# Kernel tuning notes

Measured on AMD Instinct MI355X. Metric: run time of the kernel, lower is better.

## Reference

```python
import jax, jax.numpy as jnp
import numpy as np

B, S, HIST = 2, 2048, 2048
H, HK, D = 16, 16, 128
DIM = H * D

def setup_inputs() -> dict:
    key = jax.random.key(0)
    ks = jax.random.split(key, 8)
    x = jax.random.normal(ks[0], (B, S, DIM), jnp.float32)
    prev_k = jax.random.normal(ks[1], (B, HIST, HK, D), jnp.float32)
    prev_v = jax.random.normal(ks[2], (B, HIST, HK, D), jnp.float32)
    # causal mask: history fully visible, causal within the current chunk
    q_pos = HIST + jnp.arange(S)
    k_pos = jnp.arange(HIST + S)
    mask = jnp.where(k_pos[None, :] <= q_pos[:, None], 0.0, -1e9).astype(jnp.float32)[None, None]
    sc = 0.02
    wq = jax.random.normal(ks[3], (DIM, DIM), jnp.float32) * sc
    wk = jax.random.normal(ks[4], (DIM, DIM), jnp.float32) * sc
    wv = jax.random.normal(ks[5], (DIM, DIM), jnp.float32) * sc
    wo = jax.random.normal(ks[6], (DIM, DIM), jnp.float32) * sc
    return {"x": x, "prev_k": prev_k, "prev_v": prev_v, "mask": mask,
            "wq": wq, "wk": wk, "wv": wv, "wo": wo}

def reference(x, prev_k, prev_v, mask, wq, wk, wv, wo):
    b, s, _ = x.shape
    # nn.Linear: y = x @ W^T, weights stored [out, in]
    xq = jnp.einsum('bsd,ed->bse', x, wq).reshape(b, s, H, D)
    xk = jnp.einsum('bsd,ed->bse', x, wk).reshape(b, s, HK, D)
    xv = jnp.einsum('bsd,ed->bse', x, wv).reshape(b, s, HK, D)
    k_all = jnp.concatenate([prev_k, xk], axis=1)  # [b, hist+s, hk, d]
    v_all = jnp.concatenate([prev_v, xv], axis=1)
    scores = jnp.einsum('bqhd,bkhd->bhqk', xq, k_all) / jnp.sqrt(jnp.float32(D))
    scores = scores + mask
    probs = jax.nn.softmax(scores.astype(jnp.float32), axis=-1).astype(xq.dtype)
    out = jnp.einsum('bhqk,bkhd->bqhd', probs, v_all).reshape(b, s, H * D)
    out = jnp.einsum('bse,de->bsd', out, wo)
    return out, k_all, v_all
```

## Files before the change

### kernel.cpp

```cpp
#include <hip/hip_runtime.h>
#include <math.h>

typedef __attribute__((ext_vector_type(8))) short bf16x8;
typedef __attribute__((ext_vector_type(4))) short bf16x4;
typedef __attribute__((ext_vector_type(4))) float f32x4;

#define SSCL (0.08838834764831845f * 1.4426950408889634f)

__device__ __forceinline__ short f2bf(float f) {
    union { float f; unsigned u; } x; x.f = f;
    unsigned r = x.u + 0x7fffu + ((x.u >> 16) & 1u);
    return (short)(r >> 16);
}

typedef const __attribute__((address_space(1))) unsigned int* gas_ptr;
typedef __attribute__((address_space(3))) unsigned int* las_ptr;
__device__ __forceinline__ void async_copy16(const void* g, void* l) {
    __builtin_amdgcn_global_load_lds((gas_ptr)g, (las_ptr)l, 16, 0, 0);
}

__global__ __launch_bounds__(256)
void cvt_kernel(const float* __restrict__ src, short* __restrict__ dst, int n4) {
    int i = blockIdx.x * 256 + threadIdx.x;
    const int stride = gridDim.x * 256;
    for (; i < n4; i += stride) {
        float4 v = ((const float4*)src)[i];
        bf16x4 o;
        o[0] = f2bf(v.x); o[1] = f2bf(v.y); o[2] = f2bf(v.z); o[3] = f2bf(v.w);
        ((bf16x4*)dst)[i] = o;
    }
}

__global__ __launch_bounds__(256)
void cvt3_kernel(const float* __restrict__ s0, const float* __restrict__ s1,
                 const float* __restrict__ s2, short* __restrict__ d0,
                 short* __restrict__ d1, short* __restrict__ d2, int n4) {
    const float* src = (blockIdx.y == 0) ? s0 : ((blockIdx.y == 1) ? s1 : s2);
    short* dst = (blockIdx.y == 0) ? d0 : ((blockIdx.y == 1) ? d1 : d2);
    int i = blockIdx.x * 256 + threadIdx.x;
    const int stride = gridDim.x * 256;
    for (; i < n4; i += stride) {
        float4 v = ((const float4*)src)[i];
        bf16x4 o;
        o[0] = f2bf(v.x); o[1] = f2bf(v.y); o[2] = f2bf(v.z); o[3] = f2bf(v.w);
        ((bf16x4*)dst)[i] = o;
    }
}

template<int QKV>
__global__ __launch_bounds__(256)
void gemm_kernel(const short* __restrict__ A,
                 const short* __restrict__ B0, const short* __restrict__ B1,
                 const short* __restrict__ B2,
                 short* __restrict__ D16, float* __restrict__ Dk,
                 float* __restrict__ Dv, float* __restrict__ Df) {
    __shared__ short As[128 * 64];
    __shared__ short Bs[128 * 64];
    const int tid = threadIdx.x, w = tid >> 6, ln = tid & 63;
    const int col = ln & 15, quad = ln >> 4;
    const int sel = QKV ? (blockIdx.x >> 4) : 0;
    const int tn = (blockIdx.x & 15) * 128;
    const int tm = blockIdx.y * 128;
    const short* B = (sel == 0) ? B0 : ((sel == 1) ? B1 : B2);

    const int wm = (w >> 1) * 64, wn = (w & 1) * 64;
    const int srow = ln >> 3, scol = (ln & 7) * 8;

    f32x4 acc[4][4];
    for (int i = 0; i < 4; ++i)
        for (int j = 0; j < 4; ++j)
            for (int e = 0; e < 4; ++e) acc[i][j][e] = 0.f;

    for (int k0 = 0; k0 < 2048; k0 += 64) {
        #pragma unroll
        for (int i = 0; i < 4; ++i) {
            int chunk = i * 4 + w;
            int row = chunk * 8 + srow;
            async_copy16(&A[(tm + row) * 2048 + k0 + scol], &As[chunk * 512]);
            async_copy16(&B[(tn + row) * 2048 + k0 + scol], &Bs[chunk * 512]);
        }
        asm volatile("s_waitcnt vmcnt(0)" ::: "memory");
        __syncthreads();
        #pragma unroll
        for (int kk = 0; kk < 2; ++kk) {
            bf16x8 af[4], bfr[4];
            #pragma unroll
            for (int i = 0; i < 4; ++i)
                af[i] = *(const bf16x8*)&As[(wm + i * 16 + col) * 64 + kk * 32 + quad * 8];
            #pragma unroll
            for (int j = 0; j < 4; ++j)
                bfr[j] = *(const bf16x8*)&Bs[(wn + j * 16 + col) * 64 + kk * 32 + quad * 8];
            __builtin_amdgcn_s_setprio(1);
            #pragma unroll
            for (int i = 0; i < 4; ++i)
                #pragma unroll
                for (int j = 0; j < 4; ++j)
                    acc[i][j] = __builtin_amdgcn_mfma_f32_16x16x32_bf16(af[i], bfr[j], acc[i][j], 0, 0, 0);
            __builtin_amdgcn_s_setprio(0);
        }
        __syncthreads();
    }
    for (int i = 0; i < 4; ++i)
        for (int j = 0; j < 4; ++j)
            for (int r = 0; r < 4; ++r) {
                int m = tm + wm + i * 16 + quad * 4 + r;
                int n = tn + wn + j * 16 + col;
                float v = acc[i][j][r];
                if (QKV) {
                    if (sel == 0) {
                        D16[m * 2048 + n] = f2bf(v * SSCL);
                    } else {
                        int orow = m + ((m >> 11) + 1) * 2048;
                        float* D = (sel == 1) ? Dk : Dv;
                        D[orow * 2048 + n] = v;
                    }
                } else {
                    Df[m * 2048 + n] = v;
                }
            }
}

__global__ __launch_bounds__(256)
void prep_kv(const float* __restrict__ Kall, const float* __restrict__ Vall,
             short* __restrict__ Ktg, short* __restrict__ Vtg) {
    __shared__ short L[64 * 132];
    const int tid = threadIdx.x;
    const int k0 = blockIdx.x * 64;
    const int h = blockIdx.y, b = blockIdx.z;
    const float* Kb = Kall + ((size_t)(b * 4096) * 16 + h) * 128;
    const float* Vb = Vall + ((size_t)(b * 4096) * 16 + h) * 128;
    short* Ko = Ktg + ((size_t)(b * 16 + h) * 4096) * 128;
    short* Vo = Vtg + ((size_t)(b * 16 + h) * 128) * 4096;
    #pragma unroll
    for (int i = 0; i < 8; ++i) {
        int idx = i * 256 + tid;
        int kr = idx >> 5, c4 = (idx & 31) * 4;
        float4 v = *(const float4*)&Kb[(size_t)(k0 + kr) * 2048 + c4];
        bf16x4 o4;
        o4[0] = f2bf(v.x); o4[1] = f2bf(v.y); o4[2] = f2bf(v.z); o4[3] = f2bf(v.w);
        *(bf16x4*)&Ko[(size_t)(k0 + kr) * 128 + (c4 ^ ((kr & 7) << 3))] = o4;
    }
    #pragma unroll
    for (int i = 0; i < 8; ++i) {
        int idx = i * 256 + tid;
        int r = idx >> 5, c4 = (idx & 31) * 4;
        float4 v = *(const float4*)&Vb[(size_t)(k0 + r) * 2048 + c4];
        bf16x4 o4;
        o4[0] = f2bf(v.x); o4[1] = f2bf(v.y); o4[2] = f2bf(v.z); o4[3] = f2bf(v.w);
        *(bf16x4*)&L[r * 132 + c4] = o4;
    }
    __syncthreads();
    #pragma unroll
    for (int i = 0; i < 8; ++i) {
        int idx = i * 256 + tid;
        int d = idx >> 4, kc4 = (idx & 15) * 4;
        bf16x4 o4;
        o4[0] = L[(kc4 + 0) * 132 + d];
        o4[1] = L[(kc4 + 1) * 132 + d];
        o4[2] = L[(kc4 + 2) * 132 + d];
        o4[3] = L[(kc4 + 3) * 132 + d];
        *(bf16x4*)&Vo[(size_t)d * 4096 + k0 + (kc4 ^ ((d & 7) << 3))] = o4;
    }
}

__global__ __launch_bounds__(256)
void attn_mfma(const short* __restrict__ Q, const short* __restrict__ Ktg,
               const short* __restrict__ Vtg, short* __restrict__ Ot) {
    __shared__ short Ks[2][64 * 128];
    __shared__ short Vs[2][128 * 64];
    __shared__ short Ps[4 * 16 * 72];
    const int tid = threadIdx.x, w = tid >> 6, ln = tid & 63;
    const int col = ln & 15, quad = ln >> 4;
    const int bh = blockIdx.x;
    const int b = bh >> 4, h = bh & 15;
    const int s0 = blockIdx.y * 64;
    const int xk = (col & 7) << 3;

    bf16x8 qf[4];
    {
        const int qr = (b * 2048 + s0 + w * 16 + col) * 2048 + h * 128;
        #pragma unroll
        for (int ks = 0; ks < 4; ++ks)
            qf[ks] = *(const bf16x8*)&Q[qr + ks * 32 + quad * 8];
    }
    f32x4 o[8];
    #pragma unroll
    for (int i = 0; i < 8; ++i)
        for (int e = 0; e < 4; ++e) o[i][e] = 0.f;
    float m = -1e30f, l = 0.f;

    const short* Kb = Ktg + ((size_t)(b * 16 + h) * 4096) * 128;
    const short* Vb = Vtg + ((size_t)(b * 16 + h) * 128) * 4096;
    short* PsW = &Ps[w * 1152];

    const int kr4 = ln >> 4;
    const int kc8 = (ln & 15) * 8;
    const int vd = (ln >> 3);
    const int vkofs = (ln & 7) * 8;

    const int ntiles = 33 + blockIdx.y;
    const int qp = 2048 + s0 + w * 16 + col;

    #pragma unroll
    for (int i = 0; i < 4; ++i) {
        int ch = i * 4 + w;
        async_copy16(&Kb[(size_t)(ch * 4 + kr4) * 128 + kc8], &Ks[0][ch * 512]);
        async_copy16(&Vb[(size_t)(ch * 8 + vd) * 4096 + vkofs], &Vs[0][ch * 512]);
    }
    asm volatile("s_waitcnt vmcnt(0)" ::: "memory");
    __syncthreads();

    for (int t = 0; t < ntiles; ++t) {
        const int p = t & 1;
        const int k0 = t * 64;
        const bool pf = (t + 1 < ntiles);

        if (pf) {
            const int k0n = k0 + 64;
            #pragma unroll
            for (int i = 0; i < 4; ++i) {
                int ch = i * 4 + w;
                async_copy16(&Kb[(size_t)(k0n + ch * 4 + kr4) * 128 + kc8],
                             &Ks[p ^ 1][ch * 512]);
                async_copy16(&Vb[(size_t)(ch * 8 + vd) * 4096 + k0n + vkofs],
                             &Vs[p ^ 1][ch * 512]);
            }
        }

        f32x4 s4[4];
        #pragma unroll
        for (int j = 0; j < 4; ++j)
            for (int e = 0; e < 4; ++e) s4[j][e] = 0.f;
        #pragma unroll
        for (int ks = 0; ks < 4; ++ks) {
            const int dofs = (ks * 32 + quad * 8) ^ xk;
            bf16x8 kf[4];
            #pragma unroll
            for (int j = 0; j < 4; ++j)
                kf[j] = *(const bf16x8*)&Ks[p][(j * 16 + col) * 128 + dofs];
            __builtin_amdgcn_s_setprio(1);
            #pragma unroll
            for (int j = 0; j < 4; ++j)
                s4[j] = __builtin_amdgcn_mfma_f32_16x16x32_bf16(kf[j], qf[ks], s4[j], 0, 0, 0);
            __builtin_amdgcn_s_setprio(0);
        }

        const bool full = (k0 + 63 <= 2048 + s0 + w * 16);
        float pp[4][4];
        if (full) {
            #pragma unroll
            for (int j = 0; j < 4; ++j)
                #pragma unroll
                for (int r = 0; r < 4; ++r) pp[j][r] = s4[j][r];
        } else {
            #pragma unroll
            for (int j = 0; j < 4; ++j) {
                #pragma unroll
                for (int r = 0; r < 4; ++r) {
                    int kp = k0 + j * 16 + quad * 4 + r;
                    pp[j][r] = (kp <= qp) ? s4[j][r] : -1e30f;
                }
            }
        }
        float mx = pp[0][0];
        #pragma unroll
        for (int j = 0; j < 4; ++j)
            #pragma unroll
            for (int r = 0; r < 4; ++r) mx = fmaxf(mx, pp[j][r]);
        mx = fmaxf(mx, __shfl_xor(mx, 16));
        mx = fmaxf(mx, __shfl_xor(mx, 32));

        if (__all(mx <= m)) {
            float rs = 0.f;
            #pragma unroll
            for (int j = 0; j < 4; ++j)
                #pragma unroll
                for (int r = 0; r < 4; ++r) { pp[j][r] = exp2f(pp[j][r] - m); rs += pp[j][r]; }
            rs += __shfl_xor(rs, 16);
            rs += __shfl_xor(rs, 32);
            l += rs;
        } else {
            float mn = fmaxf(m, mx);
            float al = exp2f(m - mn);
            m = mn;
            float rs = 0.f;
            #pragma unroll
            for (int j = 0; j < 4; ++j)
                #pragma unroll
                for (int r = 0; r < 4; ++r) { pp[j][r] = exp2f(pp[j][r] - mn); rs += pp[j][r]; }
            rs += __shfl_xor(rs, 16);
            rs += __shfl_xor(rs, 32);
            l = l * al + rs;
            #pragma unroll
            for (int r = 0; r < 4; ++r) {
                float alr = __shfl(al, quad * 4 + r);
                #pragma unroll
                for (int i = 0; i < 8; ++i) o[i][r] *= alr;
            }
        }

        #pragma unroll
        for (int j = 0; j < 4; ++j) {
            bf16x4 pb;
            pb[0] = f2bf(pp[j][0]); pb[1] = f2bf(pp[j][1]);
            pb[2] = f2bf(pp[j][2]); pb[3] = f2bf(pp[j][3]);
            *(bf16x4*)&PsW[col * 72 + j * 16 + quad * 4] = pb;
        }
        bf16x8 pa0 = *(const bf16x8*)&PsW[col * 72 + quad * 8];
        bf16x8 pa1 = *(const bf16x8*)&PsW[col * 72 + 32 + quad * 8];
        #pragma unroll
        for (int dt = 0; dt < 8; ++dt) {
            int row = dt * 16 + col;
            bf16x8 v0 = *(const bf16x8*)&Vs[p][row * 64 + ((quad * 8) ^ xk)];
            bf16x8 v1 = *(const bf16x8*)&Vs[p][row * 64 + ((32 + quad * 8) ^ xk)];
            __builtin_amdgcn_s_setprio(1);
            o[dt] = __builtin_amdgcn_mfma_f32_16x16x32_bf16(pa0, v0, o[dt], 0, 0, 0);
            o[dt] = __builtin_amdgcn_mfma_f32_16x16x32_bf16(pa1, v1, o[dt], 0, 0, 0);
            __builtin_amdgcn_s_setprio(0);
        }

        asm volatile("s_waitcnt vmcnt(0)" ::: "memory");
        __syncthreads();
    }
    const int orow = (b * 2048 + s0 + w * 16) * 2048 + h * 128;
    #pragma unroll
    for (int r = 0; r < 4; ++r) {
        float inv = 1.f / __shfl(l, quad * 4 + r);
        #pragma unroll
        for (int dt = 0; dt < 8; ++dt)
            Ot[orow + (quad * 4 + r) * 2048 + dt * 16 + col] = f2bf(o[dt][r] * inv);
    }
}

extern "C" void kernel_launch(void* const* d_in, const int* in_sizes, int n_in,
                              void* d_out, int out_size, void* d_ws, size_t ws_size,
                              hipStream_t stream) {
    const float* x  = (const float*)d_in[0];
    const float* pk = (const float*)d_in[1];
    const float* pv = (const float*)d_in[2];
    const float* wq = (const float*)d_in[4];
    const float* wk = (const float*)d_in[5];
    const float* wv = (const float*)d_in[6];
    const float* wo = (const float*)d_in[7];

    float* out  = (float*)d_out;
    float* kall = out + 8388608;
    float* vall = out + 25165824;

    short* ws16 = (short*)d_ws;
    short* xb  = ws16;
    short* wqb = ws16 + 8388608;
    short* wkb = ws16 + 12582912;
    short* wvb = ws16 + 16777216;
    short* wob = ws16 + 20971520;
    short* vtg = ws16 + 8388608;
    short* qbf = ws16 + 25165824;
    short* ot  = xb;
    short* ktg = (short*)out;

    hipMemcpyAsync(kall,           pk,           16777216u, hipMemcpyDeviceToDevice, stream);
    hipMemcpyAsync(kall + 8388608, pk + 4194304, 16777216u, hipMemcpyDeviceToDevice, stream);
    hipMemcpyAsync(vall,           pv,           16777216u, hipMemcpyDeviceToDevice, stream);
    hipMemcpyAsync(vall + 8388608, pv + 4194304, 16777216u, hipMemcpyDeviceToDevice, stream);

    cvt_kernel<<<1024, 256, 0, stream>>>(x, xb, 2097152);
    cvt3_kernel<<<dim3(512, 3), 256, 0, stream>>>(wq, wk, wv, wqb, wkb, wvb, 1048576);

    gemm_kernel<1><<<dim3(48, 32), 256, 0, stream>>>(xb, wqb, wkb, wvb,
                                                     qbf, kall, vall, nullptr);
    prep_kv<<<dim3(64, 16, 2), 256, 0, stream>>>(kall, vall, ktg, vtg);
    attn_mfma<<<dim3(32, 32), 256, 0, stream>>>(qbf, ktg, vtg, ot);
    cvt_kernel<<<512, 256, 0, stream>>>(wo, wob, 1048576);
    gemm_kernel<0><<<dim3(16, 32), 256, 0, stream>>>(ot, wob, wob, wob,
                                                     nullptr, nullptr, nullptr, out);
}
```

Measured before the change: 764.1 us.

## Fuse history KV copy into prep_kv and keep attention P in registers

The four device-to-device memcpys of the K/V history are removed. prep_kv now reads the history directly from prev_k/prev_v and writes the fp32 copy into the output while converting to bf16, which saves a full extra read pass over the history. In attention, P is no longer round-tripped through LDS: the PV MFMA operands are swapped (V as A, P as B) and P fragments are rearranged with lane shuffles, so the output layout becomes transposed. V becomes single-buffered with its prefetch issued after the PV stage, which frees LDS but may expose V load latency. The output now uses vectorized stores.

```diff
diff --git a/kernel.cpp b/kernel.cpp
--- a/kernel.cpp
+++ b/kernel.cpp
@@ -11,6 +11,9 @@
     union { float f; unsigned u; } x; x.f = f;
     unsigned r = x.u + 0x7fffu + ((x.u >> 16) & 1u);
     return (short)(r >> 16);
+}
+__device__ __forceinline__ unsigned pack2bf(float a, float b) {
+    return ((unsigned)(unsigned short)f2bf(a)) | (((unsigned)(unsigned short)f2bf(b)) << 16);
 }
 
 typedef const __attribute__((address_space(1))) unsigned int* gas_ptr;
@@ -121,30 +124,38 @@
 }
 
 __global__ __launch_bounds__(256)
-void prep_kv(const float* __restrict__ Kall, const float* __restrict__ Vall,
+void prep_kv(const float* __restrict__ pk, const float* __restrict__ pv,
+             float* __restrict__ Kall, float* __restrict__ Vall,
              short* __restrict__ Ktg, short* __restrict__ Vtg) {
     __shared__ short L[64 * 132];
     const int tid = threadIdx.x;
     const int k0 = blockIdx.x * 64;
     const int h = blockIdx.y, b = blockIdx.z;
-    const float* Kb = Kall + ((size_t)(b * 4096) * 16 + h) * 128;
-    const float* Vb = Vall + ((size_t)(b * 4096) * 16 + h) * 128;
-    short* Ko = Ktg + ((size_t)(b * 16 + h) * 4096) * 128;
+    const bool hist = (k0 < 2048);
+    const float* Ksrc = hist ? pk   + ((size_t)(b * 2048 + k0) * 16 + h) * 128
+                             : Kall + ((size_t)(b * 4096 + k0) * 16 + h) * 128;
+    const float* Vsrc = hist ? pv   + ((size_t)(b * 2048 + k0) * 16 + h) * 128
+                             : Vall + ((size_t)(b * 4096 + k0) * 16 + h) * 128;
+    float* Kdst = Kall + ((size_t)(b * 4096 + k0) * 16 + h) * 128;
+    float* Vdst = Vall + ((size_t)(b * 4096 + k0) * 16 + h) * 128;
+    short* Ko = Ktg + ((size_t)((b * 16 + h) * 4096) + k0) * 128;
     short* Vo = Vtg + ((size_t)(b * 16 + h) * 128) * 4096;
     #pragma unroll
     for (int i = 0; i < 8; ++i) {
         int idx = i * 256 + tid;
         int kr = idx >> 5, c4 = (idx & 31) * 4;
-        float4 v = *(const float4*)&Kb[(size_t)(k0 + kr) * 2048 + c4];
+        float4 v = *(const float4*)&Ksrc[(size_t)kr * 2048 + c4];
+        if (hist) *(float4*)&Kdst[(size_t)kr * 2048 + c4] = v;
         bf16x4 o4;
         o4[0] = f2bf(v.x); o4[1] = f2bf(v.y); o4[2] = f2bf(v.z); o4[3] = f2bf(v.w);
-        *(bf16x4*)&Ko[(size_t)(k0 + kr) * 128 + (c4 ^ ((kr & 7) << 3))] = o4;
+        *(bf16x4*)&Ko[(size_t)kr * 128 + (c4 ^ ((kr & 7) << 3))] = o4;
     }
     #pragma unroll
     for (int i = 0; i < 8; ++i) {
         int idx = i * 256 + tid;
         int r = idx >> 5, c4 = (idx & 31) * 4;
-        float4 v = *(const float4*)&Vb[(size_t)(k0 + r) * 2048 + c4];
+        float4 v = *(const float4*)&Vsrc[(size_t)r * 2048 + c4];
+        if (hist) *(float4*)&Vdst[(size_t)r * 2048 + c4] = v;
         bf16x4 o4;
         o4[0] = f2bf(v.x); o4[1] = f2bf(v.y); o4[2] = f2bf(v.z); o4[3] = f2bf(v.w);
         *(bf16x4*)&L[r * 132 + c4] = o4;
@@ -167,8 +178,7 @@
 void attn_mfma(const short* __restrict__ Q, const short* __restrict__ Ktg,
                const short* __restrict__ Vtg, short* __restrict__ Ot) {
     __shared__ short Ks[2][64 * 128];
-    __shared__ short Vs[2][128 * 64];
-    __shared__ short Ps[4 * 16 * 72];
+    __shared__ short Vs[128 * 64];
     const int tid = threadIdx.x, w = tid >> 6, ln = tid & 63;
     const int col = ln & 15, quad = ln >> 4;
     const int bh = blockIdx.x;
@@ -191,7 +201,6 @@
 
     const short* Kb = Ktg + ((size_t)(b * 16 + h) * 4096) * 128;
     const short* Vb = Vtg + ((size_t)(b * 16 + h) * 128) * 4096;
-    short* PsW = &Ps[w * 1152];
 
     const int kr4 = ln >> 4;
     const int kc8 = (ln & 15) * 8;
@@ -200,12 +209,14 @@
 
     const int ntiles = 33 + blockIdx.y;
     const int qp = 2048 + s0 + w * 16 + col;
+    const int shsrcA = col + ((quad & 1) << 5);
+    const bool qhi = (quad >> 1) != 0;
 
     #pragma unroll
     for (int i = 0; i < 4; ++i) {
         int ch = i * 4 + w;
         async_copy16(&Kb[(size_t)(ch * 4 + kr4) * 128 + kc8], &Ks[0][ch * 512]);
-        async_copy16(&Vb[(size_t)(ch * 8 + vd) * 4096 + vkofs], &Vs[0][ch * 512]);
+        async_copy16(&Vb[(size_t)(ch * 8 + vd) * 4096 + vkofs], &Vs[ch * 512]);
     }
     asm volatile("s_waitcnt vmcnt(0)" ::: "memory");
     __syncthreads();
@@ -222,8 +233,6 @@
                 int ch = i * 4 + w;
                 async_copy16(&Kb[(size_t)(k0n + ch * 4 + kr4) * 128 + kc8],
                              &Ks[p ^ 1][ch * 512]);
-                async_copy16(&Vb[(size_t)(ch * 8 + vd) * 4096 + k0n + vkofs],
-                             &Vs[p ^ 1][ch * 512]);
             }
         }
 
@@ -292,43 +301,73 @@
             rs += __shfl_xor(rs, 32);
             l = l * al + rs;
             #pragma unroll
-            for (int r = 0; r < 4; ++r) {
-                float alr = __shfl(al, quad * 4 + r);
-                #pragma unroll
-                for (int i = 0; i < 8; ++i) o[i][r] *= alr;
-            }
-        }
-
+            for (int i = 0; i < 8; ++i)
+                #pragma unroll
+                for (int r = 0; r < 4; ++r) o[i][r] *= al;
+        }
+
+        unsigned u[4][2];
         #pragma unroll
         for (int j = 0; j < 4; ++j) {
-            bf16x4 pb;
-            pb[0] = f2bf(pp[j][0]); pb[1] = f2bf(pp[j][1]);
-            pb[2] = f2bf(pp[j][2]); pb[3] = f2bf(pp[j][3]);
-            *(bf16x4*)&PsW[col * 72 + j * 16 + quad * 4] = pb;
-        }
-        bf16x8 pa0 = *(const bf16x8*)&PsW[col * 72 + quad * 8];
-        bf16x8 pa1 = *(const bf16x8*)&PsW[col * 72 + 32 + quad * 8];
+            u[j][0] = pack2bf(pp[j][0], pp[j][1]);
+            u[j][1] = pack2bf(pp[j][2], pp[j][3]);
+        }
+        unsigned pe[2][4];
+        #pragma unroll
+        for (int ks = 0; ks < 2; ++ks) {
+            const int j0 = 2 * ks, j1 = 2 * ks + 1;
+            unsigned A0 = (unsigned)__shfl((int)u[j0][0], shsrcA);
+            unsigned A1 = (unsigned)__shfl((int)u[j0][1], shsrcA);
+            unsigned A2 = (unsigned)__shfl((int)u[j1][0], shsrcA);
+            unsigned A3 = (unsigned)__shfl((int)u[j1][1], shsrcA);
+            unsigned B0 = (unsigned)__shfl((int)u[j0][0], shsrcA + 16);
+            unsigned B1 = (unsigned)__shfl((int)u[j0][1], shsrcA + 16);
+            unsigned B2 = (unsigned)__shfl((int)u[j1][0], shsrcA + 16);
+            unsigned B3 = (unsigned)__shfl((int)u[j1][1], shsrcA + 16);
+            pe[ks][0] = qhi ? A2 : A0;
+            pe[ks][1] = qhi ? A3 : A1;
+            pe[ks][2] = qhi ? B2 : B0;
+            pe[ks][3] = qhi ? B3 : B1;
+        }
+
+        asm volatile("s_waitcnt vmcnt(0)" ::: "memory");
+        __syncthreads();
+
+        union { unsigned u4[4]; bf16x8 v8; } pb0, pb1;
+        pb0.u4[0] = pe[0][0]; pb0.u4[1] = pe[0][1]; pb0.u4[2] = pe[0][2]; pb0.u4[3] = pe[0][3];
+        pb1.u4[0] = pe[1][0]; pb1.u4[1] = pe[1][1]; pb1.u4[2] = pe[1][2]; pb1.u4[3] = pe[1][3];
         #pragma unroll
         for (int dt = 0; dt < 8; ++dt) {
             int row = dt * 16 + col;
-            bf16x8 v0 = *(const bf16x8*)&Vs[p][row * 64 + ((quad * 8) ^ xk)];
-            bf16x8 v1 = *(const bf16x8*)&Vs[p][row * 64 + ((32 + quad * 8) ^ xk)];
+            bf16x8 v0 = *(const bf16x8*)&Vs[row * 64 + ((quad * 8) ^ xk)];
+            bf16x8 v1 = *(const bf16x8*)&Vs[row * 64 + ((32 + quad * 8) ^ xk)];
             __builtin_amdgcn_s_setprio(1);
-            o[dt] = __builtin_amdgcn_mfma_f32_16x16x32_bf16(pa0, v0, o[dt], 0, 0, 0);
-            o[dt] = __builtin_amdgcn_mfma_f32_16x16x32_bf16(pa1, v1, o[dt], 0, 0, 0);
+            o[dt] = __builtin_amdgcn_mfma_f32_16x16x32_bf16(v0, pb0.v8, o[dt], 0, 0, 0);
+            o[dt] = __builtin_amdgcn_mfma_f32_16x16x32_bf16(v1, pb1.v8, o[dt], 0, 0, 0);
             __builtin_amdgcn_s_setprio(0);
         }
-
-        asm volatile("s_waitcnt vmcnt(0)" ::: "memory");
         __syncthreads();
-    }
-    const int orow = (b * 2048 + s0 + w * 16) * 2048 + h * 128;
-    #pragma unroll
-    for (int r = 0; r < 4; ++r) {
-        float inv = 1.f / __shfl(l, quad * 4 + r);
-        #pragma unroll
-        for (int dt = 0; dt < 8; ++dt)
-            Ot[orow + (quad * 4 + r) * 2048 + dt * 16 + col] = f2bf(o[dt][r] * inv);
+
+        if (pf) {
+            const int k0n = k0 + 64;
+            #pragma unroll
+            for (int i = 0; i < 4; ++i) {
+                int ch = i * 4 + w;
+                async_copy16(&Vb[(size_t)(ch * 8 + vd) * 4096 + k0n + vkofs],
+                             &Vs[ch * 512]);
+            }
+        }
+    }
+    const float inv = 1.f / l;
+    const size_t ob = (size_t)(b * 2048 + s0 + w * 16 + col) * 2048 + h * 128 + quad * 4;
+    #pragma unroll
+    for (int dt = 0; dt < 8; ++dt) {
+        bf16x4 q4;
+        q4[0] = f2bf(o[dt][0] * inv);
+        q4[1] = f2bf(o[dt][1] * inv);
+        q4[2] = f2bf(o[dt][2] * inv);
+        q4[3] = f2bf(o[dt][3] * inv);
+        *(bf16x4*)&Ot[ob + dt * 16] = q4;
     }
 }
 
@@ -358,17 +397,12 @@
     short* ot  = xb;
     short* ktg = (short*)out;
 
-    hipMemcpyAsync(kall,           pk,           16777216u, hipMemcpyDeviceToDevice, stream);
-    hipMemcpyAsync(kall + 8388608, pk + 4194304, 16777216u, hipMemcpyDeviceToDevice, stream);
-    hipMemcpyAsync(vall,           pv,           16777216u, hipMemcpyDeviceToDevice, stream);
-    hipMemcpyAsync(vall + 8388608, pv + 4194304, 16777216u, hipMemcpyDeviceToDevice, stream);
-
     cvt_kernel<<<1024, 256, 0, stream>>>(x, xb, 2097152);
     cvt3_kernel<<<dim3(512, 3), 256, 0, stream>>>(wq, wk, wv, wqb, wkb, wvb, 1048576);
 
     gemm_kernel<1><<<dim3(48, 32), 256, 0, stream>>>(xb, wqb, wkb, wvb,
                                                      qbf, kall, vall, nullptr);
-    prep_kv<<<dim3(64, 16, 2), 256, 0, stream>>>(kall, vall, ktg, vtg);
+    prep_kv<<<dim3(64, 16, 2), 256, 0, stream>>>(pk, pv, kall, vall, ktg, vtg);
     attn_mfma<<<dim3(32, 32), 256, 0, stream>>>(qbf, ktg, vtg, ot);
     cvt_kernel<<<512, 256, 0, stream>>>(wo, wob, 1048576);
     gemm_kernel<0><<<dim3(16, 32), 256, 0, stream>>>(ot, wob, wob, wob,
```

New measurement: 770.5 us. Within noise of the previous version (+0.8%).
